# Kernel optimization log

Hardware: AMD Instinct MI355X
Metric: run time of the kernel (lower is better)

The kernel has to match this reference:

```python
import jax, jax.numpy as jnp
import numpy as np

N = 50000      # num nodes
E = 1_600_000  # num edges (avg degree 32)
IN = 128       # in_dim
HID = 64       # hidden_dim
H = 4          # heads (layer 1)
NEG_SLOPE = 0.2


def setup_inputs() -> dict:
    key = jax.random.key(0)
    ks = jax.random.split(key, 20)
    g = lambda k, s: jax.random.normal(k, s, dtype=jnp.float32) * 0.05
    return {
        "x": jax.random.normal(ks[0], (N, IN), dtype=jnp.float32),
        "edge_index": jax.random.randint(ks[1], (2, E), 0, N, dtype=jnp.int32),
        # GATv2 layer 1: in=128 -> heads=4, out=64, concat -> 256
        "W1l": g(ks[2], (IN, H * HID)), "b1l": g(ks[3], (H * HID,)),
        "W1r": g(ks[4], (IN, H * HID)), "b1r": g(ks[5], (H * HID,)),
        "att1": g(ks[6], (H, HID)),     "bias1": g(ks[7], (H * HID,)),
        # GATv2 layer 2: in=256 -> heads=1, out=64
        "W2l": g(ks[8], (H * HID, HID)), "b2l": g(ks[9], (HID,)),
        "W2r": g(ks[10], (H * HID, HID)), "b2r": g(ks[11], (HID,)),
        "att2": g(ks[12], (1, HID)),     "bias2": g(ks[13], (HID,)),
        # readout: 64 -> 1
        "Wro": g(ks[14], (HID, 1)), "bro": g(ks[15], (1,)),
    }


def gatv2_layer(x, src, dst, Wl, bl, Wr, br, att, bias, heads, out_ch, concat):
    n = x.shape[0]
    xl = (x @ Wl + bl).reshape(n, heads, out_ch)  # source transform [N,H,C]
    xr = (x @ Wr + br).reshape(n, heads, out_ch)  # target transform [N,H,C]
    # per-edge GATv2 score: a^T LeakyReLU(xl_j + xr_i)
    e = jax.nn.leaky_relu(xl[src] + xr[dst], NEG_SLOPE)      # [E,H,C]
    score = jnp.einsum('ehc,hc->eh', e, att)                 # [E,H]
    # segment softmax over edges sharing the same target node
    m = jax.ops.segment_max(score, dst, num_segments=n)      # [N,H]
    a = jnp.exp(score - m[dst])                              # [E,H]
    denom = jax.ops.segment_sum(a, dst, num_segments=n)      # [N,H]
    alpha = a / denom[dst]
    # weighted scatter-add of source messages
    out = jax.ops.segment_sum(xl[src] * alpha[:, :, None], dst, num_segments=n)  # [N,H,C]
    out = out.reshape(n, heads * out_ch) if concat else out.mean(axis=1)
    return out + bias


def reference(x, edge_index, W1l, b1l, W1r, b1r, att1, bias1,
              W2l, b2l, W2r, b2r, att2, bias2, Wro, bro):
    src, dst = edge_index[0], edge_index[1]
    h = gatv2_layer(x, src, dst, W1l, b1l, W1r, b1r, att1, bias1, H, HID, True)
    h = jax.nn.elu(h)
    h = gatv2_layer(h, src, dst, W2l, b2l, W2r, b2r, att2, bias2, 1, HID, True)
    h = jax.nn.elu(h)
    return h @ Wro + bro  # [N, 1]
```

## Files before the change

### kernel.cpp

```cpp
#include <hip/hip_runtime.h>
#include <hip/hip_bf16.h>
#include <cstdint>
#include <cstddef>

#define NEG_SLOPE 0.2f
#define LOG2E 1.4426950408889634f
#define NBKT 196
#define BCAP 10000
#define P1CHUNK 4096
#define P1B 391

typedef __attribute__((ext_vector_type(8))) short bf16x8;
typedef __attribute__((ext_vector_type(4))) float f32x4;

__device__ __forceinline__ unsigned short f2bf(float f) {
  unsigned u = __float_as_uint(f);
  u = u + 0x7FFFu + ((u >> 16) & 1u);
  return (unsigned short)(u >> 16);
}
__device__ __forceinline__ unsigned pack2bf(float a, float b) {
  return (unsigned)f2bf(a) | ((unsigned)f2bf(b) << 16);
}
__device__ __forceinline__ float4 cvt_bf4(uint2 q) {
  float4 v;
  v.x = __uint_as_float(q.x << 16);
  v.y = __uint_as_float(q.x & 0xffff0000u);
  v.z = __uint_as_float(q.y << 16);
  v.w = __uint_as_float(q.y & 0xffff0000u);
  return v;
}

__device__ __forceinline__ void wt_cvt(const float* __restrict__ Wl,
                                       const float* __restrict__ Wr,
                                       unsigned short* __restrict__ Wt, int K, int C, int idx) {
  const int k = idx / (2 * C);
  const int c = idx - k * 2 * C;
  const float v = (c < C) ? Wl[(size_t)k * C + c] : Wr[(size_t)k * C + (c - C)];
  Wt[(size_t)c * K + k] = f2bf(v);
}

__global__ __launch_bounds__(256) void k1_csrp1_prep(
    const int* __restrict__ src, const int* __restrict__ dst,
    int* __restrict__ bcnt, unsigned* __restrict__ stage, int E,
    const float* __restrict__ x,
    const float* __restrict__ W1l, const float* __restrict__ W1r,
    const float* __restrict__ W2l, const float* __restrict__ W2r,
    unsigned short* __restrict__ xbf, unsigned short* __restrict__ Wt1,
    unsigned short* __restrict__ Wt2, long long n8) {
  __shared__ int cnt[NBKT], gbase[NBKT];
  const int b = blockIdx.x;
  const int t = threadIdx.x;
  if (b < P1B) {
    const int base_e = b * P1CHUNK + t;
    int myd[16];
#pragma unroll
    for (int k = 0; k < 16; ++k) {
      const int e = base_e + k * 256;
      myd[k] = (e < E) ? dst[e] : -1;
    }
    for (int i = t; i < NBKT; i += 256) cnt[i] = 0;
    __syncthreads();
#pragma unroll
    for (int k = 0; k < 16; ++k)
      if (myd[k] >= 0) atomicAdd(&cnt[myd[k] >> 8], 1);
    __syncthreads();
    for (int i = t; i < NBKT; i += 256) {
      gbase[i] = cnt[i] ? atomicAdd(&bcnt[i], cnt[i]) : 0;
      cnt[i] = 0;
    }
    __syncthreads();
#pragma unroll
    for (int k = 0; k < 16; ++k) {
      const int d = myd[k];
      if (d >= 0) {
        const int bk = d >> 8;
        const int r = gbase[bk] + atomicAdd(&cnt[bk], 1);
        if (r < BCAP)
          stage[(size_t)bk * BCAP + r] =
              (unsigned)src[base_e + k * 256] | ((unsigned)(d & 255) << 24);
      }
    }
  } else if (b < P1B + 2048) {
    const int lb = b - P1B;
    long long i = (long long)lb * 256 + t;
    const long long s = 2048LL * 256;
    for (; i < n8; i += s) {
      const float4 a = ((const float4*)x)[i * 2];
      const float4 c = ((const float4*)x)[i * 2 + 1];
      ((uint2*)xbf)[i * 2] = make_uint2(pack2bf(a.x, a.y), pack2bf(a.z, a.w));
      ((uint2*)xbf)[i * 2 + 1] = make_uint2(pack2bf(c.x, c.y), pack2bf(c.z, c.w));
    }
  } else if (b < P1B + 2048 + 256) {
    wt_cvt(W1l, W1r, Wt1, 128, 256, (b - (P1B + 2048)) * 256 + t);
  } else {
    wt_cvt(W2l, W2r, Wt2, 256, 64, (b - (P1B + 2048 + 256)) * 256 + t);
  }
}

template <int K, int NT, int SPLIT>
__device__ __forceinline__ void gemm_body(
    const unsigned short* __restrict__ A, const unsigned short* __restrict__ Wt,
    const float* __restrict__ bl, const float* __restrict__ br,
    unsigned short* __restrict__ Yl, unsigned short* __restrict__ Yr, int bb) {
  constexpr int KS = K / 32;
  constexpr int CW = NT / 4;
  constexpr int NTILES = CW / 16;
  const int wv = threadIdx.x >> 6, lane = threadIdx.x & 63;
  const int n0 = bb * 16;
  const int ar = lane & 15;
  const int kg = lane >> 4;

  bf16x8 afrag[KS];
#pragma unroll
  for (int ks = 0; ks < KS; ++ks)
    afrag[ks] = *(const bf16x8*)(A + (size_t)(n0 + ar) * K + ks * 32 + kg * 8);

  const int col0w = wv * CW;
#pragma unroll
  for (int nt = 0; nt < NTILES; ++nt) {
    const int c0 = col0w + nt * 16;
    const int ccol = c0 + (lane & 15);
    f32x4 acc = {0.f, 0.f, 0.f, 0.f};
#pragma unroll
    for (int ks = 0; ks < KS; ++ks) {
      const bf16x8 bfrag = *(const bf16x8*)(Wt + (size_t)ccol * K + ks * 32 + kg * 8);
      acc = __builtin_amdgcn_mfma_f32_16x16x32_bf16(afrag[ks], bfrag, acc, 0, 0, 0);
    }
    if (c0 < SPLIT) {
      const float bv = bl[ccol];
#pragma unroll
      for (int j = 0; j < 4; ++j) {
        const int node = n0 + (lane >> 4) * 4 + j;
        Yl[(size_t)node * SPLIT + ccol] = f2bf(acc[j] + bv);
      }
    } else {
      const float bv = br[ccol - SPLIT];
#pragma unroll
      for (int j = 0; j < 4; ++j) {
        const int node = n0 + (lane >> 4) * 4 + j;
        Yr[(size_t)node * (NT - SPLIT) + (ccol - SPLIT)] = f2bf(acc[j] + bv);
      }
    }
  }
}

__global__ __launch_bounds__(256) void k2_csrp2_gemm1(
    const unsigned* __restrict__ stage, const int* __restrict__ bcnt,
    int* __restrict__ csr_src, int* __restrict__ base, int N, int E,
    const unsigned short* __restrict__ A, const unsigned short* __restrict__ Wt,
    const float* __restrict__ bl, const float* __restrict__ br,
    unsigned short* __restrict__ Yl, unsigned short* __restrict__ Yr) {
  __shared__ int h[256], c[256];
  __shared__ int allb[NBKT];
  __shared__ int ob_s;
  const int b = blockIdx.x;
  const int t = threadIdx.x;
  if (b >= NBKT) {
    gemm_body<128, 512, 256>(A, Wt, bl, br, Yl, Yr, b - NBKT);
    return;
  }
  h[t] = 0;
  for (int i = t; i < NBKT; i += 256) allb[i] = min(bcnt[i], BCAP);
  __syncthreads();
  if (t == 0) {
    int s = 0;
    for (int i = 0; i < b; ++i) s += allb[i];
    ob_s = s;
  }
  __syncthreads();
  const int out_base = ob_s;
  const int cnt = allb[b];
  const unsigned* sp = stage + (size_t)b * BCAP;
  for (int i = t; i < cnt; i += 256) atomicAdd(&h[sp[i] >> 24], 1);
  __syncthreads();
  const int own = h[t];
  for (int off = 1; off < 256; off <<= 1) {
    const int add = (t >= off) ? h[t - off] : 0;
    __syncthreads();
    h[t] += add;
    __syncthreads();
  }
  {
    const int excl = h[t] - own;
    c[t] = excl;
    const int node = b * 256 + t;
    if (node < N) base[node] = out_base + excl;
  }
  if (b == NBKT - 1 && t == 0) base[N] = E;
  __syncthreads();
  for (int i = t; i < cnt; i += 256) {
    const unsigned v = sp[i];
    const int pos = out_base + atomicAdd(&c[v >> 24], 1);
    csr_src[pos] = (int)(v & 0xFFFFFFu);
  }
}

template <int K, int NT, int SPLIT>
__global__ __launch_bounds__(256) void gemm_mfma(
    const unsigned short* __restrict__ A, const unsigned short* __restrict__ Wt,
    const float* __restrict__ bl, const float* __restrict__ br,
    unsigned short* __restrict__ Yl, unsigned short* __restrict__ Yr) {
  gemm_body<K, NT, SPLIT>(A, Wt, bl, br, Yl, Yr, blockIdx.x);
}

__device__ __forceinline__ float edge_p(const float4 c, const float4 xrv, const float4 attv) {
  const float v0 = c.x + xrv.x, v1 = c.y + xrv.y, v2 = c.z + xrv.z, v3 = c.w + xrv.w;
  float p = fmaxf(v0, v0 * NEG_SLOPE) * attv.x;
  p = fmaf(fmaxf(v1, v1 * NEG_SLOPE), attv.y, p);
  p = fmaf(fmaxf(v2, v2 * NEG_SLOPE), attv.z, p);
  p = fmaf(fmaxf(v3, v3 * NEG_SLOPE), attv.w, p);
  p += __shfl_xor(p, 1);
  p += __shfl_xor(p, 2);
  p += __shfl_xor(p, 4);
  p += __shfl_xor(p, 8);
  return __builtin_amdgcn_exp2f(p);
}

__device__ __forceinline__ void edge_acc(uint2 c, const float4& xrv, const float4& attv,
                                         float& dsum, float4& acc) {
  const float4 x = cvt_bf4(c);
  const float p = edge_p(x, xrv, attv);
  dsum += p;
  acc.x = fmaf(p, x.x, acc.x);
  acc.y = fmaf(p, x.y, acc.y);
  acc.z = fmaf(p, x.z, acc.z);
  acc.w = fmaf(p, x.w, acc.w);
}

__global__ __launch_bounds__(256) void node_l1_fused(
    const unsigned short* __restrict__ xlb, const unsigned short* __restrict__ xrb,
    const int* __restrict__ csr_src, const int* __restrict__ base,
    const float* __restrict__ att, const float* __restrict__ bias,
    unsigned short* __restrict__ outb, int N) {
  const int wv = threadIdx.x >> 6, lane = threadIdx.x & 63;
  const int n = blockIdx.x * 4 + wv;
  if (n >= N) return;
  const int beg = __builtin_amdgcn_readfirstlane(base[n]);
  const int deg = __builtin_amdgcn_readfirstlane(base[n + 1]) - beg;
  const float4 xrv = cvt_bf4(((const uint2*)xrb)[(size_t)n * 64 + lane]);
  float4 attv = ((const float4*)att)[lane];
  attv.x *= LOG2E; attv.y *= LOG2E; attv.z *= LOG2E; attv.w *= LOG2E;

  float dsum = 0.f;
  float4 acc = make_float4(0.f, 0.f, 0.f, 0.f);

  if (deg > 0) {
    const int dm1 = deg - 1;
    const char* XLc = (const char*)xlb;
    const unsigned lb = (unsigned)lane << 3;
    int s0 = csr_src[beg];
    int s1 = csr_src[beg + (1 < dm1 ? 1 : dm1)];
    int s2 = csr_src[beg + (2 < dm1 ? 2 : dm1)];
    int s3 = csr_src[beg + (3 < dm1 ? 3 : dm1)];
    uint2 r0 = *(const uint2*)(XLc + (((unsigned)s0 << 9) | lb));
    uint2 r1 = *(const uint2*)(XLc + (((unsigned)s1 << 9) | lb));
    uint2 r2 = *(const uint2*)(XLc + (((unsigned)s2 << 9) | lb));
    uint2 r3 = *(const uint2*)(XLc + (((unsigned)s3 << 9) | lb));
    s0 = csr_src[beg + (4 < dm1 ? 4 : dm1)];
    s1 = csr_src[beg + (5 < dm1 ? 5 : dm1)];
    s2 = csr_src[beg + (6 < dm1 ? 6 : dm1)];
    s3 = csr_src[beg + (7 < dm1 ? 7 : dm1)];
    for (int i = 0; i < deg; i += 4) {
      const uint2 c0 = r0, c1 = r1, c2 = r2, c3 = r3;
      r0 = *(const uint2*)(XLc + (((unsigned)s0 << 9) | lb));
      r1 = *(const uint2*)(XLc + (((unsigned)s1 << 9) | lb));
      r2 = *(const uint2*)(XLc + (((unsigned)s2 << 9) | lb));
      r3 = *(const uint2*)(XLc + (((unsigned)s3 << 9) | lb));
      const int j0 = i + 8 < dm1 ? i + 8 : dm1;
      const int j1 = i + 9 < dm1 ? i + 9 : dm1;
      const int j2 = i + 10 < dm1 ? i + 10 : dm1;
      const int j3 = i + 11 < dm1 ? i + 11 : dm1;
      s0 = csr_src[beg + j0];
      s1 = csr_src[beg + j1];
      s2 = csr_src[beg + j2];
      s3 = csr_src[beg + j3];
      edge_acc(c0, xrv, attv, dsum, acc);
      if (i + 1 <= dm1) edge_acc(c1, xrv, attv, dsum, acc);
      if (i + 2 <= dm1) edge_acc(c2, xrv, attv, dsum, acc);
      if (i + 3 <= dm1) edge_acc(c3, xrv, attv, dsum, acc);
    }
  }
  const float inv = (deg > 0) ? 1.0f / dsum : 0.f;
  const float4 b4 = ((const float4*)bias)[lane];
  float4 o;
  o.x = fmaf(acc.x, inv, b4.x); o.x = o.x > 0.f ? o.x : expm1f(o.x);
  o.y = fmaf(acc.y, inv, b4.y); o.y = o.y > 0.f ? o.y : expm1f(o.y);
  o.z = fmaf(acc.z, inv, b4.z); o.z = o.z > 0.f ? o.z : expm1f(o.z);
  o.w = fmaf(acc.w, inv, b4.w); o.w = o.w > 0.f ? o.w : expm1f(o.w);
  ((uint2*)outb)[(size_t)n * 64 + lane] = make_uint2(pack2bf(o.x, o.y), pack2bf(o.z, o.w));
}

__global__ __launch_bounds__(256) void node_l2_fused(
    const unsigned short* __restrict__ xlb, const unsigned short* __restrict__ xrb,
    const int* __restrict__ csr_src, const int* __restrict__ base,
    const float* __restrict__ att, const float* __restrict__ bias,
    const float* __restrict__ Wro, const float* __restrict__ bro,
    float* __restrict__ out, int N) {
  const int gl = threadIdx.x & 15;
  const int n = blockIdx.x * 16 + (threadIdx.x >> 4);
  const int gbase = (threadIdx.x & 63) & 48;
  if (n >= N) return;
  const int beg = base[n];
  const int deg = base[n + 1] - beg;
  const float4 xrv = cvt_bf4(((const uint2*)xrb)[(size_t)n * 16 + gl]);
  float4 attv = ((const float4*)att)[gl];
  attv.x *= LOG2E; attv.y *= LOG2E; attv.z *= LOG2E; attv.w *= LOG2E;
  const char* XLc = (const char*)xlb;
  const unsigned lb = (unsigned)gl << 3;

  float dsum = 0.f;
  float4 acc = make_float4(0.f, 0.f, 0.f, 0.f);

  for (int chunk = 0; chunk < deg; chunk += 16) {
    const int cnt = min(16, deg - chunk);
    const int si = (gl < cnt) ? csr_src[beg + chunk + gl] : 0;
    int s = __shfl(si, gbase);
    uint2 nx = *(const uint2*)(XLc + (((unsigned)s << 7) | lb));
    for (int j = 0; j < cnt; ++j) {
      const uint2 cj = nx;
      if (j + 1 < cnt) {
        const int s2 = __shfl(si, gbase + j + 1);
        nx = *(const uint2*)(XLc + (((unsigned)s2 << 7) | lb));
      }
      edge_acc(cj, xrv, attv, dsum, acc);
    }
  }
  const float inv = (deg > 0) ? 1.0f / dsum : 0.f;
  const float4 b4 = ((const float4*)bias)[gl];
  float ox = fmaf(acc.x, inv, b4.x); ox = ox > 0.f ? ox : expm1f(ox);
  float oy = fmaf(acc.y, inv, b4.y); oy = oy > 0.f ? oy : expm1f(oy);
  float oz = fmaf(acc.z, inv, b4.z); oz = oz > 0.f ? oz : expm1f(oz);
  float ow = fmaf(acc.w, inv, b4.w); ow = ow > 0.f ? ow : expm1f(ow);
  const float4 w4 = ((const float4*)Wro)[gl];
  float r = ox * w4.x + oy * w4.y + oz * w4.z + ow * w4.w;
  r += __shfl_xor(r, 1);
  r += __shfl_xor(r, 2);
  r += __shfl_xor(r, 4);
  r += __shfl_xor(r, 8);
  if (gl == 0) out[n] = r + bro[0];
}

extern "C" void kernel_launch(void* const* d_in, const int* in_sizes, int n_in,
                              void* d_out, int out_size, void* d_ws, size_t ws_size,
                              hipStream_t stream) {
  const float* x     = (const float*)d_in[0];
  const int*   ei    = (const int*)d_in[1];
  const float* W1l   = (const float*)d_in[2];
  const float* b1l   = (const float*)d_in[3];
  const float* W1r   = (const float*)d_in[4];
  const float* b1r   = (const float*)d_in[5];
  const float* att1  = (const float*)d_in[6];
  const float* bias1 = (const float*)d_in[7];
  const float* W2l   = (const float*)d_in[8];
  const float* b2l   = (const float*)d_in[9];
  const float* W2r   = (const float*)d_in[10];
  const float* b2r   = (const float*)d_in[11];
  const float* att2  = (const float*)d_in[12];
  const float* bias2 = (const float*)d_in[13];
  const float* Wro   = (const float*)d_in[14];
  const float* bro   = (const float*)d_in[15];

  const int N = in_sizes[0] / 128;
  const int E = in_sizes[1] / 2;
  const int* src = ei;
  const int* dst = ei + E;

  float* ws = (float*)d_ws;
  unsigned short* xbf  = (unsigned short*)ws;
  unsigned short* xl1b = (unsigned short*)(ws + (size_t)64 * N);
  unsigned short* xr1b = (unsigned short*)(ws + (size_t)192 * N);
  unsigned short* h1b  = (unsigned short*)(ws + (size_t)320 * N);
  int* csr_src = (int*)(ws + (size_t)448 * N);
  int* base    = csr_src + E;
  int* bcnt    = base + N + 1;
  unsigned* stage = (unsigned*)(bcnt + NBKT);
  unsigned short* Wt1 = (unsigned short*)(stage + (size_t)NBKT * BCAP);
  unsigned short* Wt2 = Wt1 + 512 * 128;
  unsigned short* xl2b = xbf;
  unsigned short* xr2b = xl1b;

  hipMemsetAsync((void*)bcnt, 0, NBKT * sizeof(int), stream);

  k1_csrp1_prep<<<dim3(P1B + 2048 + 256 + 128), dim3(256), 0, stream>>>(
      src, dst, bcnt, stage, E, x, W1l, W1r, W2l, W2r, xbf, Wt1, Wt2,
      (long long)N * 128 / 8);

  k2_csrp2_gemm1<<<dim3(NBKT + N / 16), dim3(256), 0, stream>>>(
      stage, bcnt, csr_src, base, N, E, xbf, Wt1, b1l, b1r, xl1b, xr1b);

  node_l1_fused<<<dim3((N + 3) / 4), dim3(256), 0, stream>>>(xl1b, xr1b, csr_src, base,
                                                             att1, bias1, h1b, N);

  gemm_mfma<256, 128, 64><<<dim3(N / 16), dim3(256), 0, stream>>>(h1b, Wt2, b2l, b2r,
                                                                  xl2b, xr2b);

  node_l2_fused<<<dim3((N + 15) / 16), dim3(256), 0, stream>>>(xl2b, xr2b, csr_src, base,
                                                               att2, bias2, Wro, bro,
                                                               (float*)d_out, N);
}
```

Measured before the change: 286.5 us.

## Switch intermediates to fp16 with packed-half edge scoring and DPP row reductions

Stores activations and weights as fp16 instead of bf16 and uses the f16 MFMA for both GEMMs. Per-edge scoring now does the add and LeakyReLU in packed half2 and uses fdot2 for the attention dot product. The 16-lane score reduction uses DPP row_shr adds instead of shuffles. This aims to cut ALU and cross-lane cost in the edge loops, at the price of fp16 range and precision risk for activations and scores.

```diff
diff --git a/kernel.cpp b/kernel.cpp
--- a/kernel.cpp
+++ b/kernel.cpp
@@ -1,5 +1,6 @@
 #include <hip/hip_runtime.h>
 #include <hip/hip_bf16.h>
+#include <hip/hip_fp16.h>
 #include <cstdint>
 #include <cstddef>
 
@@ -10,24 +11,29 @@
 #define P1CHUNK 4096
 #define P1B 391
 
-typedef __attribute__((ext_vector_type(8))) short bf16x8;
+typedef __attribute__((ext_vector_type(8))) _Float16 f16x8;
+typedef __attribute__((ext_vector_type(2))) _Float16 h2;
 typedef __attribute__((ext_vector_type(4))) float f32x4;
 
-__device__ __forceinline__ unsigned short f2bf(float f) {
-  unsigned u = __float_as_uint(f);
-  u = u + 0x7FFFu + ((u >> 16) & 1u);
-  return (unsigned short)(u >> 16);
-}
-__device__ __forceinline__ unsigned pack2bf(float a, float b) {
-  return (unsigned)f2bf(a) | ((unsigned)f2bf(b) << 16);
-}
-__device__ __forceinline__ float4 cvt_bf4(uint2 q) {
-  float4 v;
-  v.x = __uint_as_float(q.x << 16);
-  v.y = __uint_as_float(q.x & 0xffff0000u);
-  v.z = __uint_as_float(q.y << 16);
-  v.w = __uint_as_float(q.y & 0xffff0000u);
-  return v;
+__device__ __forceinline__ unsigned short f2h(float f) {
+  _Float16 h = (_Float16)f;
+  return __builtin_bit_cast(unsigned short, h);
+}
+__device__ __forceinline__ unsigned pack2h(float a, float b) {
+  return (unsigned)f2h(a) | ((unsigned)f2h(b) << 16);
+}
+
+template <int CTRL>
+__device__ __forceinline__ float rr_add(float x) {
+  int r = __builtin_amdgcn_update_dpp(0, __float_as_int(x), CTRL, 0xF, 0xF, false);
+  return x + __int_as_float(r);
+}
+__device__ __forceinline__ float row16_sum(float p) {
+  p = rr_add<0x121>(p);
+  p = rr_add<0x122>(p);
+  p = rr_add<0x124>(p);
+  p = rr_add<0x128>(p);
+  return p;
 }
 
 __device__ __forceinline__ void wt_cvt(const float* __restrict__ Wl,
@@ -36,7 +42,7 @@
   const int k = idx / (2 * C);
   const int c = idx - k * 2 * C;
   const float v = (c < C) ? Wl[(size_t)k * C + c] : Wr[(size_t)k * C + (c - C)];
-  Wt[(size_t)c * K + k] = f2bf(v);
+  Wt[(size_t)c * K + k] = f2h(v);
 }
 
 __global__ __launch_bounds__(256) void k1_csrp1_prep(
@@ -45,7 +51,7 @@
     const float* __restrict__ x,
     const float* __restrict__ W1l, const float* __restrict__ W1r,
     const float* __restrict__ W2l, const float* __restrict__ W2r,
-    unsigned short* __restrict__ xbf, unsigned short* __restrict__ Wt1,
+    unsigned short* __restrict__ xhf, unsigned short* __restrict__ Wt1,
     unsigned short* __restrict__ Wt2, long long n8) {
   __shared__ int cnt[NBKT], gbase[NBKT];
   const int b = blockIdx.x;
@@ -87,8 +93,8 @@
     for (; i < n8; i += s) {
       const float4 a = ((const float4*)x)[i * 2];
       const float4 c = ((const float4*)x)[i * 2 + 1];
-      ((uint2*)xbf)[i * 2] = make_uint2(pack2bf(a.x, a.y), pack2bf(a.z, a.w));
-      ((uint2*)xbf)[i * 2 + 1] = make_uint2(pack2bf(c.x, c.y), pack2bf(c.z, c.w));
+      ((uint2*)xhf)[i * 2] = make_uint2(pack2h(a.x, a.y), pack2h(a.z, a.w));
+      ((uint2*)xhf)[i * 2 + 1] = make_uint2(pack2h(c.x, c.y), pack2h(c.z, c.w));
     }
   } else if (b < P1B + 2048 + 256) {
     wt_cvt(W1l, W1r, Wt1, 128, 256, (b - (P1B + 2048)) * 256 + t);
@@ -110,10 +116,10 @@
   const int ar = lane & 15;
   const int kg = lane >> 4;
 
-  bf16x8 afrag[KS];
+  f16x8 afrag[KS];
 #pragma unroll
   for (int ks = 0; ks < KS; ++ks)
-    afrag[ks] = *(const bf16x8*)(A + (size_t)(n0 + ar) * K + ks * 32 + kg * 8);
+    afrag[ks] = *(const f16x8*)(A + (size_t)(n0 + ar) * K + ks * 32 + kg * 8);
 
   const int col0w = wv * CW;
 #pragma unroll
@@ -123,22 +129,22 @@
     f32x4 acc = {0.f, 0.f, 0.f, 0.f};
 #pragma unroll
     for (int ks = 0; ks < KS; ++ks) {
-      const bf16x8 bfrag = *(const bf16x8*)(Wt + (size_t)ccol * K + ks * 32 + kg * 8);
-      acc = __builtin_amdgcn_mfma_f32_16x16x32_bf16(afrag[ks], bfrag, acc, 0, 0, 0);
+      const f16x8 bfrag = *(const f16x8*)(Wt + (size_t)ccol * K + ks * 32 + kg * 8);
+      acc = __builtin_amdgcn_mfma_f32_16x16x32_f16(afrag[ks], bfrag, acc, 0, 0, 0);
     }
     if (c0 < SPLIT) {
       const float bv = bl[ccol];
 #pragma unroll
       for (int j = 0; j < 4; ++j) {
         const int node = n0 + (lane >> 4) * 4 + j;
-        Yl[(size_t)node * SPLIT + ccol] = f2bf(acc[j] + bv);
+        Yl[(size_t)node * SPLIT + ccol] = f2h(acc[j] + bv);
       }
     } else {
       const float bv = br[ccol - SPLIT];
 #pragma unroll
       for (int j = 0; j < 4; ++j) {
         const int node = n0 + (lane >> 4) * 4 + j;
-        Yr[(size_t)node * (NT - SPLIT) + (ccol - SPLIT)] = f2bf(acc[j] + bv);
+        Yr[(size_t)node * (NT - SPLIT) + (ccol - SPLIT)] = f2h(acc[j] + bv);
       }
     }
   }
@@ -203,50 +209,51 @@
   gemm_body<K, NT, SPLIT>(A, Wt, bl, br, Yl, Yr, blockIdx.x);
 }
 
-__device__ __forceinline__ float edge_p(const float4 c, const float4 xrv, const float4 attv) {
-  const float v0 = c.x + xrv.x, v1 = c.y + xrv.y, v2 = c.z + xrv.z, v3 = c.w + xrv.w;
-  float p = fmaxf(v0, v0 * NEG_SLOPE) * attv.x;
-  p = fmaf(fmaxf(v1, v1 * NEG_SLOPE), attv.y, p);
-  p = fmaf(fmaxf(v2, v2 * NEG_SLOPE), attv.z, p);
-  p = fmaf(fmaxf(v3, v3 * NEG_SLOPE), attv.w, p);
-  p += __shfl_xor(p, 1);
-  p += __shfl_xor(p, 2);
-  p += __shfl_xor(p, 4);
-  p += __shfl_xor(p, 8);
-  return __builtin_amdgcn_exp2f(p);
-}
-
-__device__ __forceinline__ void edge_acc(uint2 c, const float4& xrv, const float4& attv,
-                                         float& dsum, float4& acc) {
-  const float4 x = cvt_bf4(c);
-  const float p = edge_p(x, xrv, attv);
+__device__ __forceinline__ void edge_acc_h(uint2 cu, h2 xr01, h2 xr23,
+                                           h2 at01, h2 at23, h2 ns,
+                                           float& dsum, float4& acc) {
+  const h2 a01 = __builtin_bit_cast(h2, cu.x);
+  const h2 a23 = __builtin_bit_cast(h2, cu.y);
+  const h2 v01 = a01 + xr01;
+  const h2 v23 = a23 + xr23;
+  const h2 l01 = __builtin_elementwise_max(v01, v01 * ns);
+  const h2 l23 = __builtin_elementwise_max(v23, v23 * ns);
+  float p = __builtin_amdgcn_fdot2(l01, at01, 0.f, false);
+  p = __builtin_amdgcn_fdot2(l23, at23, p, false);
+  p = row16_sum(p);
+  p = __builtin_amdgcn_exp2f(p);
   dsum += p;
-  acc.x = fmaf(p, x.x, acc.x);
-  acc.y = fmaf(p, x.y, acc.y);
-  acc.z = fmaf(p, x.z, acc.z);
-  acc.w = fmaf(p, x.w, acc.w);
+  acc.x = fmaf(p, (float)a01.x, acc.x);
+  acc.y = fmaf(p, (float)a01.y, acc.y);
+  acc.z = fmaf(p, (float)a23.x, acc.z);
+  acc.w = fmaf(p, (float)a23.y, acc.w);
 }
 
 __global__ __launch_bounds__(256) void node_l1_fused(
-    const unsigned short* __restrict__ xlb, const unsigned short* __restrict__ xrb,
+    const unsigned short* __restrict__ xlh, const unsigned short* __restrict__ xrh,
     const int* __restrict__ csr_src, const int* __restrict__ base,
     const float* __restrict__ att, const float* __restrict__ bias,
-    unsigned short* __restrict__ outb, int N) {
+    unsigned short* __restrict__ outh, int N) {
   const int wv = threadIdx.x >> 6, lane = threadIdx.x & 63;
   const int n = blockIdx.x * 4 + wv;
   if (n >= N) return;
   const int beg = __builtin_amdgcn_readfirstlane(base[n]);
   const int deg = __builtin_amdgcn_readfirstlane(base[n + 1]) - beg;
-  const float4 xrv = cvt_bf4(((const uint2*)xrb)[(size_t)n * 64 + lane]);
-  float4 attv = ((const float4*)att)[lane];
-  attv.x *= LOG2E; attv.y *= LOG2E; attv.z *= LOG2E; attv.w *= LOG2E;
+  const uint2 xru = ((const uint2*)xrh)[(size_t)n * 64 + lane];
+  const h2 xr01 = __builtin_bit_cast(h2, xru.x);
+  const h2 xr23 = __builtin_bit_cast(h2, xru.y);
+  const float4 a4 = ((const float4*)att)[lane];
+  h2 at01, at23, ns;
+  at01.x = (_Float16)(a4.x * LOG2E); at01.y = (_Float16)(a4.y * LOG2E);
+  at23.x = (_Float16)(a4.z * LOG2E); at23.y = (_Float16)(a4.w * LOG2E);
+  ns.x = (_Float16)NEG_SLOPE; ns.y = (_Float16)NEG_SLOPE;
 
   float dsum = 0.f;
   float4 acc = make_float4(0.f, 0.f, 0.f, 0.f);
 
   if (deg > 0) {
     const int dm1 = deg - 1;
-    const char* XLc = (const char*)xlb;
+    const char* XLc = (const char*)xlh;
     const unsigned lb = (unsigned)lane << 3;
     int s0 = csr_src[beg];
     int s1 = csr_src[beg + (1 < dm1 ? 1 : dm1)];
@@ -274,10 +281,10 @@
       s1 = csr_src[beg + j1];
       s2 = csr_src[beg + j2];
       s3 = csr_src[beg + j3];
-      edge_acc(c0, xrv, attv, dsum, acc);
-      if (i + 1 <= dm1) edge_acc(c1, xrv, attv, dsum, acc);
-      if (i + 2 <= dm1) edge_acc(c2, xrv, attv, dsum, acc);
-      if (i + 3 <= dm1) edge_acc(c3, xrv, attv, dsum, acc);
+      edge_acc_h(c0, xr01, xr23, at01, at23, ns, dsum, acc);
+      if (i + 1 <= dm1) edge_acc_h(c1, xr01, xr23, at01, at23, ns, dsum, acc);
+      if (i + 2 <= dm1) edge_acc_h(c2, xr01, xr23, at01, at23, ns, dsum, acc);
+      if (i + 3 <= dm1) edge_acc_h(c3, xr01, xr23, at01, at23, ns, dsum, acc);
     }
   }
   const float inv = (deg > 0) ? 1.0f / dsum : 0.f;
@@ -287,11 +294,11 @@
   o.y = fmaf(acc.y, inv, b4.y); o.y = o.y > 0.f ? o.y : expm1f(o.y);
   o.z = fmaf(acc.z, inv, b4.z); o.z = o.z > 0.f ? o.z : expm1f(o.z);
   o.w = fmaf(acc.w, inv, b4.w); o.w = o.w > 0.f ? o.w : expm1f(o.w);
-  ((uint2*)outb)[(size_t)n * 64 + lane] = make_uint2(pack2bf(o.x, o.y), pack2bf(o.z, o.w));
+  ((uint2*)outh)[(size_t)n * 64 + lane] = make_uint2(pack2h(o.x, o.y), pack2h(o.z, o.w));
 }
 
 __global__ __launch_bounds__(256) void node_l2_fused(
-    const unsigned short* __restrict__ xlb, const unsigned short* __restrict__ xrb,
+    const unsigned short* __restrict__ xlh, const unsigned short* __restrict__ xrh,
     const int* __restrict__ csr_src, const int* __restrict__ base,
     const float* __restrict__ att, const float* __restrict__ bias,
     const float* __restrict__ Wro, const float* __restrict__ bro,
@@ -302,10 +309,15 @@
   if (n >= N) return;
   const int beg = base[n];
   const int deg = base[n + 1] - beg;
-  const float4 xrv = cvt_bf4(((const uint2*)xrb)[(size_t)n * 16 + gl]);
-  float4 attv = ((const float4*)att)[gl];
-  attv.x *= LOG2E; attv.y *= LOG2E; attv.z *= LOG2E; attv.w *= LOG2E;
-  const char* XLc = (const char*)xlb;
+  const uint2 xru = ((const uint2*)xrh)[(size_t)n * 16 + gl];
+  const h2 xr01 = __builtin_bit_cast(h2, xru.x);
+  const h2 xr23 = __builtin_bit_cast(h2, xru.y);
+  const float4 a4 = ((const float4*)att)[gl];
+  h2 at01, at23, ns;
+  at01.x = (_Float16)(a4.x * LOG2E); at01.y = (_Float16)(a4.y * LOG2E);
+  at23.x = (_Float16)(a4.z * LOG2E); at23.y = (_Float16)(a4.w * LOG2E);
+  ns.x = (_Float16)NEG_SLOPE; ns.y = (_Float16)NEG_SLOPE;
+  const char* XLc = (const char*)xlh;
   const unsigned lb = (unsigned)gl << 3;
 
   float dsum = 0.f;
@@ -322,7 +334,7 @@
         const int s2 = __shfl(si, gbase + j + 1);
         nx = *(const uint2*)(XLc + (((unsigned)s2 << 7) | lb));
       }
-      edge_acc(cj, xrv, attv, dsum, acc);
+      edge_acc_h(cj, xr01, xr23, at01, at23, ns, dsum, acc);
     }
   }
   const float inv = (deg > 0) ? 1.0f / dsum : 0.f;
@@ -366,35 +378,35 @@
   const int* dst = ei + E;
 
   float* ws = (float*)d_ws;
-  unsigned short* xbf  = (unsigned short*)ws;
-  unsigned short* xl1b = (unsigned short*)(ws + (size_t)64 * N);
-  unsigned short* xr1b = (unsigned short*)(ws + (size_t)192 * N);
-  unsigned short* h1b  = (unsigned short*)(ws + (size_t)320 * N);
+  unsigned short* xhf  = (unsigned short*)ws;
+  unsigned short* xl1h = (unsigned short*)(ws + (size_t)64 * N);
+  unsigned short* xr1h = (unsigned short*)(ws + (size_t)192 * N);
+  unsigned short* h1h  = (unsigned short*)(ws + (size_t)320 * N);
   int* csr_src = (int*)(ws + (size_t)448 * N);
   int* base    = csr_src + E;
   int* bcnt    = base + N + 1;
   unsigned* stage = (unsigned*)(bcnt + NBKT);
   unsigned short* Wt1 = (unsigned short*)(stage + (size_t)NBKT * BCAP);
   unsigned short* Wt2 = Wt1 + 512 * 128;
-  unsigned short* xl2b = xbf;
-  unsigned short* xr2b = xl1b;
-
-  hipMemsetAsync((void*)bcnt, 0, NBKT * sizeof(int), stream);
+  unsigned short* xl2h = xhf;
+  unsigned short* xr2h = xl1h;
+
+  (void)hipMemsetAsync((void*)bcnt, 0, NBKT * sizeof(int), stream);
 
   k1_csrp1_prep<<<dim3(P1B + 2048 + 256 + 128), dim3(256), 0, stream>>>(
-      src, dst, bcnt, stage, E, x, W1l, W1r, W2l, W2r, xbf, Wt1, Wt2,
+      src, dst, bcnt, stage, E, x, W1l, W1r, W2l, W2r, xhf, Wt1, Wt2,
       (long long)N * 128 / 8);
 
   k2_csrp2_gemm1<<<dim3(NBKT + N / 16), dim3(256), 0, stream>>>(
-      stage, bcnt, csr_src, base, N, E, xbf, Wt1, b1l, b1r, xl1b, xr1b);
-
-  node_l1_fused<<<dim3((N + 3) / 4), dim3(256), 0, stream>>>(xl1b, xr1b, csr_src, base,
-                                                             att1, bias1, h1b, N);
-
-  gemm_mfma<256, 128, 64><<<dim3(N / 16), dim3(256), 0, stream>>>(h1b, Wt2, b2l, b2r,
-                                                                  xl2b, xr2b);
-
-  node_l2_fused<<<dim3((N + 15) / 16), dim3(256), 0, stream>>>(xl2b, xr2b, csr_src, base,
+      stage, bcnt, csr_src, base, N, E, xhf, Wt1, b1l, b1r, xl1h, xr1h);
+
+  node_l1_fused<<<dim3((N + 3) / 4), dim3(256), 0, stream>>>(xl1h, xr1h, csr_src, base,
+                                                             att1, bias1, h1h, N);
+
+  gemm_mfma<256, 128, 64><<<dim3(N / 16), dim3(256), 0, stream>>>(h1h, Wt2, b2l, b2r,
+                                                                  xl2h, xr2h);
+
+  node_l2_fused<<<dim3((N + 15) / 16), dim3(256), 0, stream>>>(xl2h, xr2h, csr_src, base,
                                                                att2, bias2, Wro, bro,
                                                                (float*)d_out, N);
 }
```

Result: no change. 285.1 us (-0.5%).
